# Kernel tuning notes

Measured on AMD Instinct MI355X. Metric: run time of the kernel, lower is better.

Reference implementation:

```python
import jax, jax.numpy as jnp
import numpy as np

B, S, D, H, DH = 8192, 64, 32, 4, 8

def setup_inputs() -> dict:
    key = jax.random.key(0)
    ks = jax.random.split(key, 10)
    lim = 1.0 / np.sqrt(D)
    def lin(k):
        kw, kb = jax.random.split(k)
        W = jax.random.uniform(kw, (D, D), jnp.float32, -lim, lim)
        b = jax.random.uniform(kb, (D,), jnp.float32, -lim, lim)
        return W, b
    Wq, bq = lin(ks[0]); Wk, bk = lin(ks[1]); Wv, bv = lin(ks[2]); Wp, bp = lin(ks[3])
    x = jax.random.normal(ks[4], (B, S, D), jnp.float32)
    always_attend_upto = jax.random.randint(ks[5], (B,), 0, 64, jnp.int64 if jax.config.jax_enable_x64 else jnp.int32)
    return {"x": x, "always_attend_upto": always_attend_upto,
            "Wq": Wq, "bq": bq, "Wk": Wk, "bk": bk, "Wv": Wv, "bv": bv, "Wp": Wp, "bp": bp}

def reference(x, always_attend_upto, Wq, bq, Wk, bk, Wv, bv, Wp, bp):
    # QKV projections (torch Linear: y = x @ W.T + b)
    def heads(W, b):
        y = x @ W.T + b                      # [B,S,D]
        return y.reshape(B, S, H, DH).transpose(0, 2, 1, 3)  # [B,H,S,DH]
    q, k, v = heads(Wq, bq), heads(Wk, bk), heads(Wv, bv)
    score = jnp.einsum('bhqd,bhkd->bhqk', q, k) / jnp.sqrt(jnp.float32(DH))
    # prefix-LM mask: allowed if causal (j<=i) OR key in prefix (j < length[b])
    i = jnp.arange(S)[:, None]
    j = jnp.arange(S)[None, :]
    causal = j <= i                                        # [S,S]
    prefix = j[None, :, :] < always_attend_upto[:, None, None]  # [B,S,S]
    allowed = (causal[None] | prefix)[:, None, :, :]       # [B,1,S,S]
    score = jnp.where(allowed, score, -jnp.inf)
    attn = jax.nn.softmax(score, axis=-1)
    out = jnp.einsum('bhqk,bhkd->bhqd', attn, v)           # [B,H,S,DH]
    out = out.transpose(0, 2, 1, 3).reshape(B, S, D)
    return out @ Wp.T + bp
```

## Files before the change

kernel.cpp:

```cpp
#include <hip/hip_runtime.h>
#include <cstdint>
#include <cstddef>

#define NB 8192

typedef __attribute__((ext_vector_type(8))) short short8;
typedef __attribute__((ext_vector_type(4))) float f32x4;

union S8U { short8 s; unsigned u[4]; uint4 v; };
union FI { float f; int i; unsigned u; };

static __device__ __forceinline__ unsigned pk2(float a, float b) {
    unsigned short ua = __builtin_bit_cast(unsigned short, (__bf16)a);
    unsigned short ub = __builtin_bit_cast(unsigned short, (__bf16)b);
    return (unsigned)ua | ((unsigned)ub << 16);
}

#define MFMA __builtin_amdgcn_mfma_f32_16x16x32_bf16
#define BPERM __builtin_amdgcn_ds_bpermute

__global__ __launch_bounds__(128, 5) void fused_attn_mfma(
    const float* __restrict__ x,
    const int*   __restrict__ aatt,
    const float* __restrict__ Wq, const float* __restrict__ bq,
    const float* __restrict__ Wk, const float* __restrict__ bk,
    const float* __restrict__ Wv, const float* __restrict__ bv,
    const float* __restrict__ Wp, const float* __restrict__ bp,
    float* __restrict__ out)
{
    __shared__ __align__(16) short klds[64][40];
    __shared__ __align__(16) short vbt[33][72];

    const int tid  = threadIdx.x;
    const int w    = tid >> 6;
    const int lane = tid & 63;
    const int q4   = lane >> 4;
    const int l15  = lane & 15;
    const int b    = blockIdx.x;

    const int aab = aatt[b];
    const unsigned bmask = (q4 == 0) ? 0xFFFFFFFFu : 0u;

    int cmpv[4];
#pragma unroll
    for (int it = 0; it < 4; ++it) cmpv[it] = max(l15 + 16*it, aab - 1) - q4*4;

    short8 xa[4];
    const float* xb = x + (size_t)b * 64 * 32;
#pragma unroll
    for (int nt = 0; nt < 4; ++nt) {
        const float* p = xb + (nt*16 + l15)*32 + q4*8;
        float4 u0 = *(const float4*)p;
        float4 u1 = *(const float4*)(p + 4);
        S8U t;
        t.u[0] = pk2(u0.x, u0.y); t.u[1] = pk2(u0.z, u0.w);
        t.u[2] = pk2(u1.x, u1.y); t.u[3] = pk2(u1.z, u1.w);
        xa[nt] = t.s;
    }

    auto wrow = [&](const float* W, int row) -> short8 {
        const float* p = W + row*32 + q4*8;
        float4 u0 = *(const float4*)p;
        float4 u1 = *(const float4*)(p + 4);
        S8U t;
        t.u[0] = pk2(u0.x, u0.y); t.u[1] = pk2(u0.z, u0.w);
        t.u[2] = pk2(u1.x, u1.y); t.u[3] = pk2(u1.z, u1.w);
        return t.s;
    };

    const float escale = 0.35355339059327373f * 1.4426950408889634f;

    unsigned qpk01[4], qpk23[4];
    {
        short8 wa = wrow(Wq, 16*w + l15);
        float4 b4 = *(const float4*)(bq + 16*w + q4*4);
#pragma unroll
        for (int nt = 0; nt < 4; ++nt) {
            f32x4 acc = {0.f,0.f,0.f,0.f};
            acc = MFMA(wa, xa[nt], acc, 0,0,0);
            qpk01[nt] = pk2((acc[0]+b4.x)*escale, (acc[1]+b4.y)*escale);
            qpk23[nt] = pk2((acc[2]+b4.z)*escale, (acc[3]+b4.w)*escale);
        }
    }
    {
        short8 wa = wrow(Wk, 16*w + l15);
        float4 b4 = *(const float4*)(bk + 16*w + q4*4);
#pragma unroll
        for (int nt = 0; nt < 4; ++nt) {
            f32x4 acc = {0.f,0.f,0.f,0.f};
            acc = MFMA(wa, xa[nt], acc, 0,0,0);
            uint2 w2;
            w2.x = pk2(acc[0]+b4.x, acc[1]+b4.y);
            w2.y = pk2(acc[2]+b4.z, acc[3]+b4.w);
            *(uint2*)&klds[nt*16 + l15][16*w + q4*4] = w2;
        }
    }
    {
        short8 wv = wrow(Wv, 16*w + l15);
        const float bvv = bv[16*w + l15];
#pragma unroll
        for (int mt = 0; mt < 4; ++mt) {
            f32x4 acc = {0.f,0.f,0.f,0.f};
            acc = MFMA(xa[mt], wv, acc, 0,0,0);
            uint2 w2;
            w2.x = pk2(acc[0]+bvv, acc[1]+bvv);
            w2.y = pk2(acc[2]+bvv, acc[3]+bvv);
            *(uint2*)&vbt[16*w + l15][(mt >> 1)*32 + q4*8 + (mt & 1)*4] = w2;
        }
    }
    if (q4 == 0) {
        uint2 ones; ones.x = 0x3F803F80u; ones.y = 0x3F803F80u;
        *(uint2*)&vbt[32][l15*4] = ones;
    }

#pragma unroll
    for (int hl = 0; hl < 2; ++hl) {
        const int idxA = (32*hl + l15) * 4;
        const int idxB = idxA + 64;

        short8 sqb[4];
#pragma unroll
        for (int it = 0; it < 4; ++it) {
            S8U t;
            t.u[0] = (unsigned)BPERM(idxA, (int)qpk01[it]) & bmask;
            t.u[1] = (unsigned)BPERM(idxA, (int)qpk23[it]) & bmask;
            t.u[2] = (unsigned)BPERM(idxB, (int)qpk01[it]) & bmask;
            t.u[3] = (unsigned)BPERM(idxB, (int)qpk23[it]) & bmask;
            sqb[it] = t.s;
        }

        const int avrow = (l15 < 8) ? (16*w + 8*hl + l15) : 32;

        f32x4 oacch[4];
#pragma unroll
        for (int it = 0; it < 4; ++it) oacch[it] = (f32x4){0.f,0.f,0.f,0.f};

#pragma unroll
        for (int jb = 0; jb < 2; ++jb) {
            S8U ska0, ska1, av;
            ska0.v = *(const uint4*)&klds[jb*32 + l15][16*w + 8*hl];
            ska1.v = *(const uint4*)&klds[jb*32 + 16 + l15][16*w + 8*hl];
            av.v   = *(const uint4*)&vbt[avrow][jb*32 + q4*8];

#pragma unroll
            for (int it = 0; it < 4; ++it) {
                S8U pb;
                {
                    f32x4 sacc = {0.f,0.f,0.f,0.f};
                    sacc = MFMA(ska0.s, sqb[it], sacc, 0,0,0);
                    float e[4];
#pragma unroll
                    for (int r = 0; r < 4; ++r) {
                        float ee = __builtin_amdgcn_exp2f(sacc[r]);
                        e[r] = (jb*32 + r <= cmpv[it]) ? ee : 0.0f;
                    }
                    pb.u[0] = pk2(e[0], e[1]); pb.u[1] = pk2(e[2], e[3]);
                }
                {
                    f32x4 sacc = {0.f,0.f,0.f,0.f};
                    sacc = MFMA(ska1.s, sqb[it], sacc, 0,0,0);
                    float e[4];
#pragma unroll
                    for (int r = 0; r < 4; ++r) {
                        float ee = __builtin_amdgcn_exp2f(sacc[r]);
                        e[r] = (jb*32 + 16 + r <= cmpv[it]) ? ee : 0.0f;
                    }
                    pb.u[2] = pk2(e[0], e[1]); pb.u[3] = pk2(e[2], e[3]);
                }
                oacch[it] = MFMA(av.s, pb.s, oacch[it], 0,0,0);
            }
        }

#pragma unroll
        for (int it = 0; it < 4; ++it) {
            FI s; s.i = BPERM((32 + l15) * 4, __builtin_bit_cast(int, oacch[it][0]));
            const float inv = __builtin_amdgcn_rcpf(s.f);
            const unsigned o01 = pk2(oacch[it][0]*inv, oacch[it][1]*inv);
            const unsigned o23 = pk2(oacch[it][2]*inv, oacch[it][3]*inv);
            if (q4 < 2) {
                uint2 ow; ow.x = o01; ow.y = o23;
                *(uint2*)&klds[it*16 + l15][(2*w + hl)*8 + q4*4] = ow;
            }
        }
    }

    __syncthreads();

    short8 wpb[2];
#pragma unroll
    for (int nt = 0; nt < 2; ++nt) wpb[nt] = wrow(Wp, nt*16 + l15);

    const float bpv[2] = { bp[l15], bp[16 + l15] };
    float* ob = out + (size_t)b * 64 * 32;
#pragma unroll
    for (int u = 0; u < 2; ++u) {
        S8U oa; oa.v = *(const uint4*)&klds[(2*w + u)*16 + l15][q4*8];
#pragma unroll
        for (int nt = 0; nt < 2; ++nt) {
            f32x4 y = {0.f,0.f,0.f,0.f};
            y = MFMA(oa.s, wpb[nt], y, 0,0,0);
#pragma unroll
            for (int r = 0; r < 4; ++r)
                ob[((2*w + u)*16 + q4*4 + r)*32 + nt*16 + l15] = y[r] + bpv[nt];
        }
    }
}

extern "C" void kernel_launch(void* const* d_in, const int* in_sizes, int n_in,
                              void* d_out, int out_size, void* d_ws, size_t ws_size,
                              hipStream_t stream) {
    const float* x  = (const float*)d_in[0];
    const int*   aa = (const int*)d_in[1];
    const float* Wq = (const float*)d_in[2];
    const float* bq = (const float*)d_in[3];
    const float* Wk = (const float*)d_in[4];
    const float* bk = (const float*)d_in[5];
    const float* Wv = (const float*)d_in[6];
    const float* bv = (const float*)d_in[7];
    const float* Wp = (const float*)d_in[8];
    const float* bp = (const float*)d_in[9];
    float* out = (float*)d_out;

    dim3 grid(NB), block(128);
    hipLaunchKernelGGL(fused_attn_mfma, grid, block, 0, stream,
                       x, aa, Wq, bq, Wk, bk, Wv, bv, Wp, bp, out);
}
```

Measured before the change: 50.68 us.

## Process four batches per block, hoisting weight loads out of batch loop

Each block now loops over four batch elements, and the grid shrinks to a quarter. The Wq/Wk/Wv/Wp rows and biases are loaded and converted to bf16 once per block rather than once per batch, and the ones-row setup is hoisted out of the loop. A second barrier is added at the end of each iteration so LDS can be reused. The cost is serialized work per block, fewer blocks to hide latency, an extra sync per batch, more live registers, and a lower occupancy hint in launch bounds (5 to 4).

```diff
diff --git a/kernel.cpp b/kernel.cpp
--- a/kernel.cpp
+++ b/kernel.cpp
@@ -3,6 +3,7 @@
 #include <cstddef>
 
 #define NB 8192
+#define NBPB 4
 
 typedef __attribute__((ext_vector_type(8))) short short8;
 typedef __attribute__((ext_vector_type(4))) float f32x4;
@@ -19,7 +20,7 @@
 #define MFMA __builtin_amdgcn_mfma_f32_16x16x32_bf16
 #define BPERM __builtin_amdgcn_ds_bpermute
 
-__global__ __launch_bounds__(128, 5) void fused_attn_mfma(
+__global__ __launch_bounds__(128, 4) void fused_attn_mfma(
     const float* __restrict__ x,
     const int*   __restrict__ aatt,
     const float* __restrict__ Wq, const float* __restrict__ bq,
@@ -36,27 +37,8 @@
     const int lane = tid & 63;
     const int q4   = lane >> 4;
     const int l15  = lane & 15;
-    const int b    = blockIdx.x;
-
-    const int aab = aatt[b];
+
     const unsigned bmask = (q4 == 0) ? 0xFFFFFFFFu : 0u;
-
-    int cmpv[4];
-#pragma unroll
-    for (int it = 0; it < 4; ++it) cmpv[it] = max(l15 + 16*it, aab - 1) - q4*4;
-
-    short8 xa[4];
-    const float* xb = x + (size_t)b * 64 * 32;
-#pragma unroll
-    for (int nt = 0; nt < 4; ++nt) {
-        const float* p = xb + (nt*16 + l15)*32 + q4*8;
-        float4 u0 = *(const float4*)p;
-        float4 u1 = *(const float4*)(p + 4);
-        S8U t;
-        t.u[0] = pk2(u0.x, u0.y); t.u[1] = pk2(u0.z, u0.w);
-        t.u[2] = pk2(u1.x, u1.y); t.u[3] = pk2(u1.z, u1.w);
-        xa[nt] = t.s;
-    }
 
     auto wrow = [&](const float* W, int row) -> short8 {
         const float* p = W + row*32 + q4*8;
@@ -70,139 +52,159 @@
 
     const float escale = 0.35355339059327373f * 1.4426950408889634f;
 
-    unsigned qpk01[4], qpk23[4];
-    {
-        short8 wa = wrow(Wq, 16*w + l15);
-        float4 b4 = *(const float4*)(bq + 16*w + q4*4);
+    const short8 wq8 = wrow(Wq, 16*w + l15);
+    const short8 wk8 = wrow(Wk, 16*w + l15);
+    const short8 wv8 = wrow(Wv, 16*w + l15);
+    const float4 bq4 = *(const float4*)(bq + 16*w + q4*4);
+    const float4 bk4 = *(const float4*)(bk + 16*w + q4*4);
+    const float  bvv = bv[16*w + l15];
+    short8 wpb[2];
+    wpb[0] = wrow(Wp, l15);
+    wpb[1] = wrow(Wp, 16 + l15);
+    const float bpv[2] = { bp[l15], bp[16 + l15] };
+
+    if (q4 == 0) {
+        uint2 ones; ones.x = 0x3F803F80u; ones.y = 0x3F803F80u;
+        *(uint2*)&vbt[32][l15*4] = ones;
+    }
+
+#pragma unroll 1
+    for (int bi = 0; bi < NBPB; ++bi) {
+        const int b = blockIdx.x * NBPB + bi;
+        const int aab = aatt[b];
+
+        int cmpv[4];
+#pragma unroll
+        for (int it = 0; it < 4; ++it) cmpv[it] = max(l15 + 16*it, aab - 1) - q4*4;
+
+        short8 xa[4];
+        const float* xb = x + (size_t)b * 64 * 32;
+#pragma unroll
+        for (int nt = 0; nt < 4; ++nt) {
+            const float* p = xb + (nt*16 + l15)*32 + q4*8;
+            float4 u0 = *(const float4*)p;
+            float4 u1 = *(const float4*)(p + 4);
+            S8U t;
+            t.u[0] = pk2(u0.x, u0.y); t.u[1] = pk2(u0.z, u0.w);
+            t.u[2] = pk2(u1.x, u1.y); t.u[3] = pk2(u1.z, u1.w);
+            xa[nt] = t.s;
+        }
+
+        unsigned qpk01[4], qpk23[4];
 #pragma unroll
         for (int nt = 0; nt < 4; ++nt) {
             f32x4 acc = {0.f,0.f,0.f,0.f};
-            acc = MFMA(wa, xa[nt], acc, 0,0,0);
-            qpk01[nt] = pk2((acc[0]+b4.x)*escale, (acc[1]+b4.y)*escale);
-            qpk23[nt] = pk2((acc[2]+b4.z)*escale, (acc[3]+b4.w)*escale);
-        }
-    }
-    {
-        short8 wa = wrow(Wk, 16*w + l15);
-        float4 b4 = *(const float4*)(bk + 16*w + q4*4);
+            acc = MFMA(wq8, xa[nt], acc, 0,0,0);
+            qpk01[nt] = pk2((acc[0]+bq4.x)*escale, (acc[1]+bq4.y)*escale);
+            qpk23[nt] = pk2((acc[2]+bq4.z)*escale, (acc[3]+bq4.w)*escale);
+        }
 #pragma unroll
         for (int nt = 0; nt < 4; ++nt) {
             f32x4 acc = {0.f,0.f,0.f,0.f};
-            acc = MFMA(wa, xa[nt], acc, 0,0,0);
+            acc = MFMA(wk8, xa[nt], acc, 0,0,0);
             uint2 w2;
-            w2.x = pk2(acc[0]+b4.x, acc[1]+b4.y);
-            w2.y = pk2(acc[2]+b4.z, acc[3]+b4.w);
+            w2.x = pk2(acc[0]+bk4.x, acc[1]+bk4.y);
+            w2.y = pk2(acc[2]+bk4.z, acc[3]+bk4.w);
             *(uint2*)&klds[nt*16 + l15][16*w + q4*4] = w2;
         }
-    }
-    {
-        short8 wv = wrow(Wv, 16*w + l15);
-        const float bvv = bv[16*w + l15];
 #pragma unroll
         for (int mt = 0; mt < 4; ++mt) {
             f32x4 acc = {0.f,0.f,0.f,0.f};
-            acc = MFMA(xa[mt], wv, acc, 0,0,0);
+            acc = MFMA(xa[mt], wv8, acc, 0,0,0);
             uint2 w2;
             w2.x = pk2(acc[0]+bvv, acc[1]+bvv);
             w2.y = pk2(acc[2]+bvv, acc[3]+bvv);
             *(uint2*)&vbt[16*w + l15][(mt >> 1)*32 + q4*8 + (mt & 1)*4] = w2;
         }
-    }
-    if (q4 == 0) {
-        uint2 ones; ones.x = 0x3F803F80u; ones.y = 0x3F803F80u;
-        *(uint2*)&vbt[32][l15*4] = ones;
-    }
-
-#pragma unroll
-    for (int hl = 0; hl < 2; ++hl) {
-        const int idxA = (32*hl + l15) * 4;
-        const int idxB = idxA + 64;
-
-        short8 sqb[4];
-#pragma unroll
-        for (int it = 0; it < 4; ++it) {
-            S8U t;
-            t.u[0] = (unsigned)BPERM(idxA, (int)qpk01[it]) & bmask;
-            t.u[1] = (unsigned)BPERM(idxA, (int)qpk23[it]) & bmask;
-            t.u[2] = (unsigned)BPERM(idxB, (int)qpk01[it]) & bmask;
-            t.u[3] = (unsigned)BPERM(idxB, (int)qpk23[it]) & bmask;
-            sqb[it] = t.s;
-        }
-
-        const int avrow = (l15 < 8) ? (16*w + 8*hl + l15) : 32;
-
-        f32x4 oacch[4];
-#pragma unroll
-        for (int it = 0; it < 4; ++it) oacch[it] = (f32x4){0.f,0.f,0.f,0.f};
-
-#pragma unroll
-        for (int jb = 0; jb < 2; ++jb) {
-            S8U ska0, ska1, av;
-            ska0.v = *(const uint4*)&klds[jb*32 + l15][16*w + 8*hl];
-            ska1.v = *(const uint4*)&klds[jb*32 + 16 + l15][16*w + 8*hl];
-            av.v   = *(const uint4*)&vbt[avrow][jb*32 + q4*8];
-
+
+#pragma unroll
+        for (int hl = 0; hl < 2; ++hl) {
+            const int idxA = (32*hl + l15) * 4;
+            const int idxB = idxA + 64;
+
+            short8 sqb[4];
 #pragma unroll
             for (int it = 0; it < 4; ++it) {
-                S8U pb;
-                {
-                    f32x4 sacc = {0.f,0.f,0.f,0.f};
-                    sacc = MFMA(ska0.s, sqb[it], sacc, 0,0,0);
-                    float e[4];
-#pragma unroll
-                    for (int r = 0; r < 4; ++r) {
-                        float ee = __builtin_amdgcn_exp2f(sacc[r]);
-                        e[r] = (jb*32 + r <= cmpv[it]) ? ee : 0.0f;
+                S8U t;
+                t.u[0] = (unsigned)BPERM(idxA, (int)qpk01[it]) & bmask;
+                t.u[1] = (unsigned)BPERM(idxA, (int)qpk23[it]) & bmask;
+                t.u[2] = (unsigned)BPERM(idxB, (int)qpk01[it]) & bmask;
+                t.u[3] = (unsigned)BPERM(idxB, (int)qpk23[it]) & bmask;
+                sqb[it] = t.s;
+            }
+
+            const int avrow = (l15 < 8) ? (16*w + 8*hl + l15) : 32;
+
+            f32x4 oacch[4];
+#pragma unroll
+            for (int it = 0; it < 4; ++it) oacch[it] = (f32x4){0.f,0.f,0.f,0.f};
+
+#pragma unroll
+            for (int jb = 0; jb < 2; ++jb) {
+                S8U ska0, ska1, av;
+                ska0.v = *(const uint4*)&klds[jb*32 + l15][16*w + 8*hl];
+                ska1.v = *(const uint4*)&klds[jb*32 + 16 + l15][16*w + 8*hl];
+                av.v   = *(const uint4*)&vbt[avrow][jb*32 + q4*8];
+
+#pragma unroll
+                for (int it = 0; it < 4; ++it) {
+                    S8U pb;
+                    {
+                        f32x4 sacc = {0.f,0.f,0.f,0.f};
+                        sacc = MFMA(ska0.s, sqb[it], sacc, 0,0,0);
+                        float e[4];
+#pragma unroll
+                        for (int r = 0; r < 4; ++r) {
+                            float ee = __builtin_amdgcn_exp2f(sacc[r]);
+                            e[r] = (jb*32 + r <= cmpv[it]) ? ee : 0.0f;
+                        }
+                        pb.u[0] = pk2(e[0], e[1]); pb.u[1] = pk2(e[2], e[3]);
                     }
-                    pb.u[0] = pk2(e[0], e[1]); pb.u[1] = pk2(e[2], e[3]);
+                    {
+                        f32x4 sacc = {0.f,0.f,0.f,0.f};
+                        sacc = MFMA(ska1.s, sqb[it], sacc, 0,0,0);
+                        float e[4];
+#pragma unroll
+                        for (int r = 0; r < 4; ++r) {
+                            float ee = __builtin_amdgcn_exp2f(sacc[r]);
+                            e[r] = (jb*32 + 16 + r <= cmpv[it]) ? ee : 0.0f;
+                        }
+                        pb.u[2] = pk2(e[0], e[1]); pb.u[3] = pk2(e[2], e[3]);
+                    }
+                    oacch[it] = MFMA(av.s, pb.s, oacch[it], 0,0,0);
                 }
-                {
-                    f32x4 sacc = {0.f,0.f,0.f,0.f};
-                    sacc = MFMA(ska1.s, sqb[it], sacc, 0,0,0);
-                    float e[4];
-#pragma unroll
-                    for (int r = 0; r < 4; ++r) {
-                        float ee = __builtin_amdgcn_exp2f(sacc[r]);
-                        e[r] = (jb*32 + 16 + r <= cmpv[it]) ? ee : 0.0f;
-                    }
-                    pb.u[2] = pk2(e[0], e[1]); pb.u[3] = pk2(e[2], e[3]);
+            }
+
+#pragma unroll
+            for (int it = 0; it < 4; ++it) {
+                FI s; s.i = BPERM((32 + l15) * 4, __builtin_bit_cast(int, oacch[it][0]));
+                const float inv = __builtin_amdgcn_rcpf(s.f);
+                const unsigned o01 = pk2(oacch[it][0]*inv, oacch[it][1]*inv);
+                const unsigned o23 = pk2(oacch[it][2]*inv, oacch[it][3]*inv);
+                if (q4 < 2) {
+                    uint2 ow; ow.x = o01; ow.y = o23;
+                    *(uint2*)&klds[it*16 + l15][(2*w + hl)*8 + q4*4] = ow;
                 }
-                oacch[it] = MFMA(av.s, pb.s, oacch[it], 0,0,0);
-            }
-        }
-
-#pragma unroll
-        for (int it = 0; it < 4; ++it) {
-            FI s; s.i = BPERM((32 + l15) * 4, __builtin_bit_cast(int, oacch[it][0]));
-            const float inv = __builtin_amdgcn_rcpf(s.f);
-            const unsigned o01 = pk2(oacch[it][0]*inv, oacch[it][1]*inv);
-            const unsigned o23 = pk2(oacch[it][2]*inv, oacch[it][3]*inv);
-            if (q4 < 2) {
-                uint2 ow; ow.x = o01; ow.y = o23;
-                *(uint2*)&klds[it*16 + l15][(2*w + hl)*8 + q4*4] = ow;
-            }
-        }
-    }
-
-    __syncthreads();
-
-    short8 wpb[2];
-#pragma unroll
-    for (int nt = 0; nt < 2; ++nt) wpb[nt] = wrow(Wp, nt*16 + l15);
-
-    const float bpv[2] = { bp[l15], bp[16 + l15] };
-    float* ob = out + (size_t)b * 64 * 32;
-#pragma unroll
-    for (int u = 0; u < 2; ++u) {
-        S8U oa; oa.v = *(const uint4*)&klds[(2*w + u)*16 + l15][q4*8];
-#pragma unroll
-        for (int nt = 0; nt < 2; ++nt) {
-            f32x4 y = {0.f,0.f,0.f,0.f};
-            y = MFMA(oa.s, wpb[nt], y, 0,0,0);
-#pragma unroll
-            for (int r = 0; r < 4; ++r)
-                ob[((2*w + u)*16 + q4*4 + r)*32 + nt*16 + l15] = y[r] + bpv[nt];
-        }
+            }
+        }
+
+        __syncthreads();
+
+        float* ob = out + (size_t)b * 64 * 32;
+#pragma unroll
+        for (int u = 0; u < 2; ++u) {
+            S8U oa; oa.v = *(const uint4*)&klds[(2*w + u)*16 + l15][q4*8];
+#pragma unroll
+            for (int nt = 0; nt < 2; ++nt) {
+                f32x4 y = {0.f,0.f,0.f,0.f};
+                y = MFMA(oa.s, wpb[nt], y, 0,0,0);
+#pragma unroll
+                for (int r = 0; r < 4; ++r)
+                    ob[((2*w + u)*16 + q4*4 + r)*32 + nt*16 + l15] = y[r] + bpv[nt];
+            }
+        }
+
+        __syncthreads();
     }
 }
 
@@ -221,7 +223,7 @@
     const float* bp = (const float*)d_in[9];
     float* out = (float*)d_out;
 
-    dim3 grid(NB), block(128);
+    dim3 grid(NB / NBPB), block(128);
     hipLaunchKernelGGL(fused_attn_mfma, grid, block, 0, stream,
                        x, aa, Wq, bq, Wk, bk, Wv, bv, Wp, bp, out);
 }
```

After: 51.65 us. Within noise of the previous version (+1.9%).

## Process all four heads in one wavefront per batch and drop block barrier

Applied to the files above, without the earlier changes.

The block shrinks from two wavefronts, each handling two heads, to a single 64-lane wavefront that computes the Q/K/V projections and attention for all four heads. It then runs the output projection for all 64 rows itself. This removes the duplicated per-wave load and conversion of x, and removes the __syncthreads before the output projection. In exchange each wave does twice the MFMA and exp work and holds more registers. LDS per block is unchanged, so fewer waves may be resident per CU to hide memory latency.

```diff
diff --git a/kernel.cpp b/kernel.cpp
--- a/kernel.cpp
+++ b/kernel.cpp
@@ -19,7 +19,7 @@
 #define MFMA __builtin_amdgcn_mfma_f32_16x16x32_bf16
 #define BPERM __builtin_amdgcn_ds_bpermute
 
-__global__ __launch_bounds__(128, 5) void fused_attn_mfma(
+__global__ __launch_bounds__(64) void fused_attn_mfma(
     const float* __restrict__ x,
     const int*   __restrict__ aatt,
     const float* __restrict__ Wq, const float* __restrict__ bq,
@@ -31,9 +31,7 @@
     __shared__ __align__(16) short klds[64][40];
     __shared__ __align__(16) short vbt[33][72];
 
-    const int tid  = threadIdx.x;
-    const int w    = tid >> 6;
-    const int lane = tid & 63;
+    const int lane = threadIdx.x;
     const int q4   = lane >> 4;
     const int l15  = lane & 15;
     const int b    = blockIdx.x;
@@ -70,21 +68,23 @@
 
     const float escale = 0.35355339059327373f * 1.4426950408889634f;
 
-    unsigned qpk01[4], qpk23[4];
-    {
-        short8 wa = wrow(Wq, 16*w + l15);
-        float4 b4 = *(const float4*)(bq + 16*w + q4*4);
+    unsigned qpk01[2][4], qpk23[2][4];
+#pragma unroll
+    for (int mt = 0; mt < 2; ++mt) {
+        short8 wa = wrow(Wq, mt*16 + l15);
+        float4 b4 = *(const float4*)(bq + mt*16 + q4*4);
 #pragma unroll
         for (int nt = 0; nt < 4; ++nt) {
             f32x4 acc = {0.f,0.f,0.f,0.f};
             acc = MFMA(wa, xa[nt], acc, 0,0,0);
-            qpk01[nt] = pk2((acc[0]+b4.x)*escale, (acc[1]+b4.y)*escale);
-            qpk23[nt] = pk2((acc[2]+b4.z)*escale, (acc[3]+b4.w)*escale);
-        }
-    }
-    {
-        short8 wa = wrow(Wk, 16*w + l15);
-        float4 b4 = *(const float4*)(bk + 16*w + q4*4);
+            qpk01[mt][nt] = pk2((acc[0]+b4.x)*escale, (acc[1]+b4.y)*escale);
+            qpk23[mt][nt] = pk2((acc[2]+b4.z)*escale, (acc[3]+b4.w)*escale);
+        }
+    }
+#pragma unroll
+    for (int mt = 0; mt < 2; ++mt) {
+        short8 wa = wrow(Wk, mt*16 + l15);
+        float4 b4 = *(const float4*)(bk + mt*16 + q4*4);
 #pragma unroll
         for (int nt = 0; nt < 4; ++nt) {
             f32x4 acc = {0.f,0.f,0.f,0.f};
@@ -92,12 +92,13 @@
             uint2 w2;
             w2.x = pk2(acc[0]+b4.x, acc[1]+b4.y);
             w2.y = pk2(acc[2]+b4.z, acc[3]+b4.w);
-            *(uint2*)&klds[nt*16 + l15][16*w + q4*4] = w2;
-        }
-    }
-    {
-        short8 wv = wrow(Wv, 16*w + l15);
-        const float bvv = bv[16*w + l15];
+            *(uint2*)&klds[nt*16 + l15][mt*16 + q4*4] = w2;
+        }
+    }
+#pragma unroll
+    for (int nt = 0; nt < 2; ++nt) {
+        short8 wv = wrow(Wv, nt*16 + l15);
+        const float bvv = bv[nt*16 + l15];
 #pragma unroll
         for (int mt = 0; mt < 4; ++mt) {
             f32x4 acc = {0.f,0.f,0.f,0.f};
@@ -105,7 +106,7 @@
             uint2 w2;
             w2.x = pk2(acc[0]+bvv, acc[1]+bvv);
             w2.y = pk2(acc[2]+bvv, acc[3]+bvv);
-            *(uint2*)&vbt[16*w + l15][(mt >> 1)*32 + q4*8 + (mt & 1)*4] = w2;
+            *(uint2*)&vbt[nt*16 + l15][(mt >> 1)*32 + q4*8 + (mt & 1)*4] = w2;
         }
     }
     if (q4 == 0) {
@@ -114,22 +115,24 @@
     }
 
 #pragma unroll
-    for (int hl = 0; hl < 2; ++hl) {
-        const int idxA = (32*hl + l15) * 4;
+    for (int h = 0; h < 4; ++h) {
+        const int mth = h >> 1;
+        const int p   = h & 1;
+        const int idxA = (32*p + l15) * 4;
         const int idxB = idxA + 64;
 
         short8 sqb[4];
 #pragma unroll
         for (int it = 0; it < 4; ++it) {
             S8U t;
-            t.u[0] = (unsigned)BPERM(idxA, (int)qpk01[it]) & bmask;
-            t.u[1] = (unsigned)BPERM(idxA, (int)qpk23[it]) & bmask;
-            t.u[2] = (unsigned)BPERM(idxB, (int)qpk01[it]) & bmask;
-            t.u[3] = (unsigned)BPERM(idxB, (int)qpk23[it]) & bmask;
+            t.u[0] = (unsigned)BPERM(idxA, (int)qpk01[mth][it]) & bmask;
+            t.u[1] = (unsigned)BPERM(idxA, (int)qpk23[mth][it]) & bmask;
+            t.u[2] = (unsigned)BPERM(idxB, (int)qpk01[mth][it]) & bmask;
+            t.u[3] = (unsigned)BPERM(idxB, (int)qpk23[mth][it]) & bmask;
             sqb[it] = t.s;
         }
 
-        const int avrow = (l15 < 8) ? (16*w + 8*hl + l15) : 32;
+        const int avrow = (l15 < 8) ? (8*h + l15) : 32;
 
         f32x4 oacch[4];
 #pragma unroll
@@ -138,8 +141,8 @@
 #pragma unroll
         for (int jb = 0; jb < 2; ++jb) {
             S8U ska0, ska1, av;
-            ska0.v = *(const uint4*)&klds[jb*32 + l15][16*w + 8*hl];
-            ska1.v = *(const uint4*)&klds[jb*32 + 16 + l15][16*w + 8*hl];
+            ska0.v = *(const uint4*)&klds[jb*32 + l15][8*h];
+            ska1.v = *(const uint4*)&klds[jb*32 + 16 + l15][8*h];
             av.v   = *(const uint4*)&vbt[avrow][jb*32 + q4*8];
 
 #pragma unroll
@@ -179,29 +182,27 @@
             const unsigned o23 = pk2(oacch[it][2]*inv, oacch[it][3]*inv);
             if (q4 < 2) {
                 uint2 ow; ow.x = o01; ow.y = o23;
-                *(uint2*)&klds[it*16 + l15][(2*w + hl)*8 + q4*4] = ow;
+                *(uint2*)&klds[it*16 + l15][8*h + q4*4] = ow;
             }
         }
     }
 
-    __syncthreads();
-
     short8 wpb[2];
-#pragma unroll
-    for (int nt = 0; nt < 2; ++nt) wpb[nt] = wrow(Wp, nt*16 + l15);
-
+    wpb[0] = wrow(Wp, l15);
+    wpb[1] = wrow(Wp, 16 + l15);
     const float bpv[2] = { bp[l15], bp[16 + l15] };
+
     float* ob = out + (size_t)b * 64 * 32;
 #pragma unroll
-    for (int u = 0; u < 2; ++u) {
-        S8U oa; oa.v = *(const uint4*)&klds[(2*w + u)*16 + l15][q4*8];
+    for (int it = 0; it < 4; ++it) {
+        S8U oa; oa.v = *(const uint4*)&klds[it*16 + l15][q4*8];
 #pragma unroll
         for (int nt = 0; nt < 2; ++nt) {
             f32x4 y = {0.f,0.f,0.f,0.f};
             y = MFMA(oa.s, wpb[nt], y, 0,0,0);
 #pragma unroll
             for (int r = 0; r < 4; ++r)
-                ob[((2*w + u)*16 + q4*4 + r)*32 + nt*16 + l15] = y[r] + bpv[nt];
+                ob[(it*16 + q4*4 + r)*32 + nt*16 + l15] = y[r] + bpv[nt];
         }
     }
 }
@@ -221,7 +222,7 @@
     const float* bp = (const float*)d_in[9];
     float* out = (float*)d_out;
 
-    dim3 grid(NB), block(128);
+    dim3 grid(NB), block(64);
     hipLaunchKernelGGL(fused_attn_mfma, grid, block, 0, stream,
                        x, aa, Wq, bq, Wk, bk, Wv, bv, Wp, bp, out);
 }
```

New measurement: 57.51 us. 1.13x slower.
